# Optimization experiments

Hardware: AMD Instinct MI355X
Metric: run time of the kernel (lower is better)

## Reference

```python
import jax, jax.numpy as jnp
import numpy as np

N = 100000          # n_nodes
E = 1600000         # n_edges (avg degree 16)
IN = 256            # in_dim
OUT = 16            # out_dim
SLOPE = 0.2         # leaky_relu negative slope
DROP = 0.5          # dropout rate


def _xavier(key, shape):
    fan_in, fan_out = shape
    std = (2.0 / (fan_in + fan_out)) ** 0.5
    return std * jax.random.normal(key, shape, jnp.float32)


def setup_inputs() -> dict:
    key = jax.random.key(0)
    ks = jax.random.split(key, 10)
    x = jax.random.normal(ks[0], (N, IN), jnp.float32)
    row = jax.random.randint(ks[1], (E,), 0, N, jnp.int32)
    col = jax.random.randint(ks[2], (E,), 0, N, jnp.int32)
    edge_w = jax.random.uniform(ks[3], (E,), jnp.float32)
    W1 = _xavier(ks[4], (IN, IN // 2)); b1 = jnp.zeros((IN // 2,), jnp.float32)
    W2 = _xavier(ks[5], (IN // 2, IN // 4)); b2 = jnp.zeros((IN // 4,), jnp.float32)
    W3 = _xavier(ks[6], (IN // 4, IN // 8)); b3 = jnp.zeros((IN // 8,), jnp.float32)
    W4 = _xavier(ks[7], (IN // 8, OUT)); b4 = jnp.zeros((OUT,), jnp.float32)
    # dropout mask (training-mode dropout made deterministic; pre-scaled by 1/(1-p))
    drop_mask = (jax.random.uniform(ks[8], (N, IN // 2)) > DROP).astype(jnp.float32) / (1.0 - DROP)
    return dict(x=x, row=row, col=col, edge_w=edge_w,
                W1=W1, b1=b1, W2=W2, b2=b2, W3=W3, b3=b3, W4=W4, b4=b4,
                drop_mask=drop_mask)


def reference(x, row, col, edge_w, W1, b1, W2, b2, W3, b3, W4, b4, drop_mask):
    def spmm(h):
        # out[i] = sum over edges (i <- j): w_ij * h[j]   (sparse adj @ h)
        return jax.ops.segment_sum(edge_w[:, None] * h[col], row, num_segments=N)

    lrelu = lambda v: jax.nn.leaky_relu(v, SLOPE)

    h = spmm(x @ W1) + b1          # gc1: [N, IN/2]
    h = lrelu(h) * drop_mask       # leaky_relu + dropout
    h = spmm(h @ W2) + b2          # gc2: [N, IN/4]
    h = lrelu(h)
    h = lrelu(h @ W3 + b3)         # clf hidden: [N, IN/8]
    return h @ W4 + b4             # logits: [N, OUT]
```

## Files before the change

### kernel.cpp

```cpp
#include <hip/hip_runtime.h>
#include <hip/hip_bf16.h>

#define N_NODES 100000
#define N_EDGES 1600000
#define SLOPE_ 0.2f
#define NBK 196
#define BCAP 9216
#define NCB 13
#define KEYS (512 * NCB)
#define BINBLK 256
#define PREPBLK 1583

typedef __attribute__((ext_vector_type(8))) short bf16x8;
typedef __attribute__((ext_vector_type(4))) float f32x4;

__device__ __forceinline__ short f2bf(float f) {
    __hip_bfloat16 h = __float2bfloat16(f);
    return *reinterpret_cast<short*>(&h);
}
__device__ __forceinline__ float bflo(unsigned u) { return __uint_as_float(u << 16); }
__device__ __forceinline__ float bfhi(unsigned u) { return __uint_as_float(u & 0xFFFF0000u); }
__device__ __forceinline__ float bf2f(short s) {
    return __uint_as_float(((unsigned)(unsigned short)s) << 16);
}


__global__ void zero_k(int* __restrict__ cur) {
    int t = threadIdx.x;
    if (t < NBK) cur[t] = 0;
}


__global__ void passA_k(const int* __restrict__ row, const int* __restrict__ col,
                        const float* __restrict__ ew, int* __restrict__ cur,
                        int2* __restrict__ binned,
                        const float* __restrict__ W1, const float* __restrict__ W2,
                        const float* __restrict__ mask,
                        short* __restrict__ Bp1, short* __restrict__ Bp2,
                        unsigned* __restrict__ mp) {
    __shared__ int hist[NBK], base[NBK], off[NBK];
    int t = threadIdx.x;
    if (blockIdx.x < BINBLK) {
        const int chunk = N_EDGES / BINBLK;
        int e0 = blockIdx.x * chunk;
        for (int i = t; i < NBK; i += 256) { hist[i] = 0; off[i] = 0; }
        __syncthreads();
        for (int i = t; i < chunk; i += 256) {
            int b = row[e0 + i] >> 9;
            atomicAdd(&hist[b], 1);
        }
        __syncthreads();
        for (int i = t; i < NBK; i += 256)
            base[i] = atomicAdd(&cur[i], hist[i]);
        __syncthreads();
        for (int i = t; i < chunk; i += 256) {
            int e = e0 + i;
            int r = row[e], c = col[e];
            int b = r >> 9;
            int p = base[b] + atomicAdd(&off[b], 1);
            if (p < BCAP)
                binned[(size_t)b * BCAP + p] =
                    make_int2(((r & 511) << 17) | c, __float_as_int(ew[e]));
        }
        return;
    }
    int i = (blockIdx.x - BINBLK) * 256 + t;
    if (i < 4096) {
        int ln = i & 15, nt = (i >> 4) & 7, g = (i >> 7) & 3, ks = i >> 9;
        int n = nt * 16 + ln, k0 = ks * 32 + g * 8;
        bf16x8 v;
#pragma unroll
        for (int j = 0; j < 8; j++) v[j] = f2bf(W1[(k0 + j) * 128 + n]);
        *(bf16x8*)(Bp1 + (size_t)i * 8) = v;
    } else if (i < 5120) {
        int c = i - 4096;
        int ln = c & 15, nt = (c >> 4) & 3, g = (c >> 6) & 3, ks = c >> 8;
        int n = nt * 16 + ln, k0 = ks * 32 + g * 8;
        bf16x8 v;
#pragma unroll
        for (int j = 0; j < 8; j++) v[j] = f2bf(W2[(k0 + j) * 64 + n]);
        *(bf16x8*)(Bp2 + (size_t)c * 8) = v;
    } else {
        int wi = i - 5120;
        if (wi < N_NODES * 4) {
            const float4* p = (const float4*)(mask + (size_t)wi * 32);
            unsigned b = 0;
#pragma unroll
            for (int j = 0; j < 8; j++) {
                float4 v = p[j];
                b |= (unsigned)(v.x != 0.f) << (4 * j);
                b |= (unsigned)(v.y != 0.f) << (4 * j + 1);
                b |= (unsigned)(v.z != 0.f) << (4 * j + 2);
                b |= (unsigned)(v.w != 0.f) << (4 * j + 3);
            }
            mp[wi] = b;
        }
    }
}


__global__ void __launch_bounds__(512) passB_k(const int2* __restrict__ binned,
                                               const int* __restrict__ cur,
                                               unsigned* __restrict__ cw,
                                               int* __restrict__ row_ptr) {
    __shared__ int hist[KEYS];
    __shared__ int offs[KEYS];
    __shared__ int ssum[512];
    __shared__ int bexc[256];
    int t = threadIdx.x, b = blockIdx.x;
    const int2* src = binned + (size_t)b * BCAP;
    int cnt = cur[b];
    if (cnt > BCAP) cnt = BCAP;

    if (t < 256) bexc[t] = (t < NBK) ? min(cur[t], BCAP) : 0;
    __syncthreads();
    for (int off2 = 1; off2 < 256; off2 <<= 1) {
        int v = (t < 256 && t >= off2) ? bexc[t - off2] : 0;
        __syncthreads();
        if (t < 256) bexc[t] += v;
        __syncthreads();
    }
    int gbase = bexc[b] - cnt;

    for (int i = t; i < KEYS; i += 512) hist[i] = 0;
    __syncthreads();

    for (int i = t; i < cnt; i += 512) {
        int2 v = src[i];
        int c = v.x & 0x1FFFF, lr = v.x >> 17;
        atomicAdd(&hist[lr * NCB + (c >> 13)], 1);
    }
    __syncthreads();

    int loc[NCB];
    int tot = 0;
#pragma unroll
    for (int j = 0; j < NCB; j++) {
        loc[j] = tot;
        tot += hist[t * NCB + j];
    }
    ssum[t] = tot;
    __syncthreads();
    for (int off2 = 1; off2 < 512; off2 <<= 1) {
        int v = (t >= off2) ? ssum[t - off2] : 0;
        __syncthreads();
        ssum[t] += v;
        __syncthreads();
    }
    int base = ssum[t] - tot;
#pragma unroll
    for (int j = 0; j < NCB; j++) offs[t * NCB + j] = base + loc[j];

    int grow = b * 512 + t;
    if (grow <= N_NODES) row_ptr[grow] = gbase + base;
    __syncthreads();

    for (int i = t; i < cnt; i += 512) {
        int2 v = src[i];
        int c = v.x & 0x1FFFF, lr = v.x >> 17;
        int p = gbase + atomicAdd(&offs[lr * NCB + (c >> 13)], 1);
        unsigned wb = (unsigned)(unsigned short)f2bf(__int_as_float(v.y));
        cw[p] = ((unsigned)c << 15) | (wb & 0x7FFFu);
    }
}


template <int K, int COLS, bool ABF16>
__global__ __launch_bounds__(512) void gemm_p(const void* __restrict__ Ap,
                                              const short* __restrict__ Bp,
                                              short* __restrict__ out, int M) {
    constexpr int NT = COLS / 16;
    constexpr int NKS = K / 32;
    __shared__ short Bs[K * COLS];
    int t = threadIdx.x;
    for (int i = t; i < K * COLS / 8; i += 512)
        *(bf16x8*)(Bs + (size_t)i * 8) = *(const bf16x8*)(Bp + (size_t)i * 8);
    __syncthreads();

    int l = t & 63, wv = t >> 6;
    int ln = l & 15, g = l >> 4;
    int row0 = blockIdx.x * 256 + wv * 32;
    int r0 = row0 + ln, r1 = row0 + 16 + ln;
    int cr0 = min(r0, M - 1), cr1 = min(r1, M - 1);

    f32x4 acc[2][NT];
#pragma unroll
    for (int rf = 0; rf < 2; rf++)
#pragma unroll
        for (int nt = 0; nt < NT; nt++) acc[rf][nt] = (f32x4){0.f, 0.f, 0.f, 0.f};

#pragma unroll
    for (int ks = 0; ks < NKS; ks++) {
        int kk = ks * 32 + g * 8;
        bf16x8 a0, a1;
        if constexpr (ABF16) {
            a0 = *(const bf16x8*)((const short*)Ap + (size_t)cr0 * K + kk);
            a1 = *(const bf16x8*)((const short*)Ap + (size_t)cr1 * K + kk);
        } else {
            const float* p0 = (const float*)Ap + (size_t)cr0 * K + kk;
            const float* p1 = (const float*)Ap + (size_t)cr1 * K + kk;
            float4 u0 = *(const float4*)p0;
            float4 u1 = *(const float4*)(p0 + 4);
            float4 v0 = *(const float4*)p1;
            float4 v1 = *(const float4*)(p1 + 4);
            a0[0] = f2bf(u0.x); a0[1] = f2bf(u0.y); a0[2] = f2bf(u0.z); a0[3] = f2bf(u0.w);
            a0[4] = f2bf(u1.x); a0[5] = f2bf(u1.y); a0[6] = f2bf(u1.z); a0[7] = f2bf(u1.w);
            a1[0] = f2bf(v0.x); a1[1] = f2bf(v0.y); a1[2] = f2bf(v0.z); a1[3] = f2bf(v0.w);
            a1[4] = f2bf(v1.x); a1[5] = f2bf(v1.y); a1[6] = f2bf(v1.z); a1[7] = f2bf(v1.w);
        }
#pragma unroll
        for (int nt = 0; nt < NT; nt++) {
            bf16x8 b = *(const bf16x8*)(Bs + (size_t)((((ks * 4 + g) * NT + nt) * 16 + ln)) * 8);
            acc[0][nt] = __builtin_amdgcn_mfma_f32_16x16x32_bf16(a0, b, acc[0][nt], 0, 0, 0);
            acc[1][nt] = __builtin_amdgcn_mfma_f32_16x16x32_bf16(a1, b, acc[1][nt], 0, 0, 0);
        }
    }
#pragma unroll
    for (int rf = 0; rf < 2; rf++)
#pragma unroll
        for (int nt = 0; nt < NT; nt++)
#pragma unroll
            for (int r = 0; r < 4; r++) {
                int orow = row0 + rf * 16 + g * 4 + r;
                if (orow < M) out[(size_t)orow * COLS + nt * 16 + ln] = f2bf(acc[rf][nt][r]);
            }
}


template <int D, bool DROP>
__global__ void spmm_bf(const int* __restrict__ row_ptr, const unsigned* __restrict__ cwp,
                        const short* __restrict__ h,
                        const float* __restrict__ bias, const unsigned* __restrict__ maskp,
                        short* __restrict__ out, int n) {
    int bid = blockIdx.x;
    int sbid = (bid & 7) * 3125 + (bid >> 3);
    int wid = sbid * 4 + (int)(threadIdx.x >> 6);
    int lane = threadIdx.x & 63;
    if (wid >= n) return;
    int sp = __builtin_amdgcn_readfirstlane(row_ptr[wid]);
    int ep = __builtin_amdgcn_readfirstlane(row_ptr[wid + 1]);
    int cnt = ep - sp;
    const unsigned* pcw = cwp + sp;
    const unsigned* hb = (const unsigned*)h;
    float ax = 0.f, ay = 0.f;

    if (D == 128) {
        for (int jb = 0; jb < cnt; jb += 8) {
            unsigned u[8];
            float w[8];
#pragma unroll
            for (int p = 0; p < 8; p++) {
                int idx = jb + p;
                unsigned md = pcw[idx];
                md = (idx < cnt) ? md : 0u;
                int c = (int)(md >> 15);
                w[p] = __uint_as_float((md & 0x7FFFu) << 16);
                u[p] = hb[(size_t)c * 64 + lane];
            }
#pragma unroll
            for (int p = 0; p < 8; p++) {
                ax += w[p] * bflo(u[p]);
                ay += w[p] * bfhi(u[p]);
            }
        }
        float2 b = *(const float2*)(bias + 2 * lane);
        float ox = ax + b.x, oy = ay + b.y;
        ox = ox > 0.f ? ox : SLOPE_ * ox;
        oy = oy > 0.f ? oy : SLOPE_ * oy;
        if (DROP) {
            unsigned mw = maskp[(size_t)wid * 4 + (lane >> 4)];
            unsigned sh = (2 * lane) & 31;
            ox = ((mw >> sh) & 1u) ? 2.f * ox : 0.f;
            oy = ((mw >> (sh + 1)) & 1u) ? 2.f * oy : 0.f;
        }
        unsigned ov = (unsigned)(unsigned short)f2bf(ox) |
                      ((unsigned)(unsigned short)f2bf(oy) << 16);
        *(unsigned*)(out + (size_t)wid * 128 + 2 * lane) = ov;
    } else {
        int li = lane & 31;
        for (int jb = 0; jb < cnt; jb += 8) {
            unsigned u[4];
            float w[4];
#pragma unroll
            for (int p = 0; p < 4; p++) {
                int iA = jb + 2 * p, iB = iA + 1;
                unsigned mA = pcw[iA];
                mA = (iA < cnt) ? mA : 0u;
                unsigned mB = pcw[iB];
                mB = (iB < cnt) ? mB : 0u;
                unsigned md = (lane < 32) ? mA : mB;
                int c = (int)(md >> 15);
                w[p] = __uint_as_float((md & 0x7FFFu) << 16);
                u[p] = hb[(size_t)c * 32 + li];
            }
#pragma unroll
            for (int p = 0; p < 4; p++) {
                ax += w[p] * bflo(u[p]);
                ay += w[p] * bfhi(u[p]);
            }
        }
        ax += __shfl_xor(ax, 32);
        ay += __shfl_xor(ay, 32);
        float2 b = *(const float2*)(bias + li * 2);
        float ox = ax + b.x, oy = ay + b.y;
        ox = ox > 0.f ? ox : SLOPE_ * ox;
        oy = oy > 0.f ? oy : SLOPE_ * oy;
        unsigned ov = (unsigned)(unsigned short)f2bf(ox) |
                      ((unsigned)(unsigned short)f2bf(oy) << 16);
        if (lane < 32) *(unsigned*)(out + (size_t)wid * 64 + li * 2) = ov;
    }
}


__global__ void clf_k(const short* __restrict__ h, const float* __restrict__ W3,
                      const float* __restrict__ b3, const float* __restrict__ W4,
                      const float* __restrict__ b4, float* __restrict__ out) {
    __shared__ float W3s[64][32];
    __shared__ float W4s[32][16];
    __shared__ float b3s[32], b4s[16];
    __shared__ float hs[32][64];
    __shared__ float t4[32][33];
    int t = threadIdx.x;
    for (int l = t; l < 64 * 32; l += 256) W3s[l / 32][l % 32] = W3[l];
    for (int l = t; l < 32 * 16; l += 256) W4s[l / 16][l % 16] = W4[l];
    if (t < 32) b3s[t] = b3[t];
    if (t < 16) b4s[t] = b4[t];
    int row0 = blockIdx.x * 32;
    {
        bf16x8 v = *(const bf16x8*)(h + (size_t)row0 * 64 + t * 8);
        int r = t >> 3, c0 = (t & 7) << 3;
#pragma unroll
        for (int j = 0; j < 8; j++) hs[r][c0 + j] = bf2f(v[j]);
    }
    __syncthreads();
    for (int l = t; l < 1024; l += 256) {
        int r = l / 32, c = l % 32;
        float a = b3s[c];
#pragma unroll 8
        for (int k = 0; k < 64; k++) a += hs[r][k] * W3s[k][c];
        t4[r][c] = a > 0.f ? a : SLOPE_ * a;
    }
    __syncthreads();
    for (int l = t; l < 512; l += 256) {
        int r = l / 16, c = l % 16;
        float a = b4s[c];
#pragma unroll
        for (int k = 0; k < 32; k++) a += t4[r][k] * W4s[k][c];
        out[(size_t)(row0 + r) * 16 + c] = a;
    }
}


extern "C" void kernel_launch(void* const* d_in, const int* in_sizes, int n_in,
                              void* d_out, int out_size, void* d_ws, size_t ws_size,
                              hipStream_t stream) {
    const float* x = (const float*)d_in[0];
    const int* row = (const int*)d_in[1];
    const int* col = (const int*)d_in[2];
    const float* ew = (const float*)d_in[3];
    const float* W1 = (const float*)d_in[4];
    const float* b1 = (const float*)d_in[5];
    const float* W2 = (const float*)d_in[6];
    const float* b2 = (const float*)d_in[7];
    const float* W3 = (const float*)d_in[8];
    const float* b3 = (const float*)d_in[9];
    const float* W4 = (const float*)d_in[10];
    const float* b4 = (const float*)d_in[11];
    const float* mask = (const float*)d_in[12];
    float* out = (float*)d_out;

    const int N = N_NODES, E = N_EDGES;

    short* h0 = (short*)d_ws;
    short* h1 = h0 + (size_t)N * 128;
    short* h2 = h1 + (size_t)N * 128;
    short* h3 = h2 + (size_t)N * 64;
    short* Bp1 = h3 + (size_t)N * 64;
    short* Bp2 = Bp1 + 32768;
    int* row_ptr = (int*)(Bp2 + 8192);
    int* cur = row_ptr + N + 1;
    unsigned* mask_p = (unsigned*)(cur + NBK + 3);
    unsigned* cwp = mask_p + (size_t)N * 4;
    int2* binned = (int2*)h0;

    zero_k<<<1, 256, 0, stream>>>(cur);
    passA_k<<<BINBLK + PREPBLK, 256, 0, stream>>>(row, col, ew, cur, binned,
                                                  W1, W2, mask, Bp1, Bp2, mask_p);
    passB_k<<<NBK, 512, 0, stream>>>(binned, cur, cwp, row_ptr);

    gemm_p<256, 128, false><<<(N + 255) / 256, 512, 0, stream>>>(x, Bp1, h0, N);
    spmm_bf<128, true><<<25000, 256, 0, stream>>>(row_ptr, cwp, h0, b1, mask_p, h1, N);
    gemm_p<128, 64, true><<<(N + 255) / 256, 512, 0, stream>>>(h1, Bp2, h2, N);
    spmm_bf<64, false><<<25000, 256, 0, stream>>>(row_ptr, cwp, h2, b2, nullptr, h3, N);
    clf_k<<<N / 32, 256, 0, stream>>>(h3, W3, b3, W4, b4, out);
}
```

Before: 225.1 us.

## Shard bin counters into 8 groups and pack dropout mask with wave ballot

Edge binning now keeps 8 per-group counters and sub-buckets per row bin instead of one global counter per bin. This spreads global atomic contention across more addresses, and passB merges the groups when building the CSR. The dropout-mask bit packing is rewritten to use coalesced per-lane float loads plus a wave-wide ballot that writes 64 bits at once, replacing strided float4 loads per thread. Per-group capacity (1280) is tighter than before, so a skewed bin could overflow and drop edges.

```diff
diff --git a/kernel.cpp b/kernel.cpp
--- a/kernel.cpp
+++ b/kernel.cpp
@@ -5,11 +5,14 @@
 #define N_EDGES 1600000
 #define SLOPE_ 0.2f
 #define NBK 196
+#define NGRP 8
+#define BCAPG 1280
 #define BCAP 9216
 #define NCB 13
 #define KEYS (512 * NCB)
 #define BINBLK 256
-#define PREPBLK 1583
+#define PREPW 20
+#define PMBLK 1563
 
 typedef __attribute__((ext_vector_type(8))) short bf16x8;
 typedef __attribute__((ext_vector_type(4))) float f32x4;
@@ -25,82 +28,83 @@
 }
 
 
-__global__ void zero_k(int* __restrict__ cur) {
-    int t = threadIdx.x;
-    if (t < NBK) cur[t] = 0;
+__global__ void zero_k(int* __restrict__ cur8) {
+    for (int i = threadIdx.x; i < NBK * NGRP; i += 256) cur8[i] = 0;
 }
 
 
 __global__ void passA_k(const int* __restrict__ row, const int* __restrict__ col,
-                        const float* __restrict__ ew, int* __restrict__ cur,
+                        const float* __restrict__ ew, int* __restrict__ cur8,
                         int2* __restrict__ binned,
                         const float* __restrict__ W1, const float* __restrict__ W2,
                         const float* __restrict__ mask,
                         short* __restrict__ Bp1, short* __restrict__ Bp2,
                         unsigned* __restrict__ mp) {
-    __shared__ int hist[NBK], base[NBK], off[NBK];
     int t = threadIdx.x;
     if (blockIdx.x < BINBLK) {
+        __shared__ int hist[NBK], base[NBK], off[NBK];
+        int g = blockIdx.x & (NGRP - 1);
         const int chunk = N_EDGES / BINBLK;
         int e0 = blockIdx.x * chunk;
         for (int i = t; i < NBK; i += 256) { hist[i] = 0; off[i] = 0; }
         __syncthreads();
-        for (int i = t; i < chunk; i += 256) {
-            int b = row[e0 + i] >> 9;
-            atomicAdd(&hist[b], 1);
-        }
+        for (int i = t; i < chunk; i += 256)
+            atomicAdd(&hist[row[e0 + i] >> 9], 1);
         __syncthreads();
         for (int i = t; i < NBK; i += 256)
-            base[i] = atomicAdd(&cur[i], hist[i]);
+            base[i] = atomicAdd(&cur8[i * NGRP + g], hist[i]);
         __syncthreads();
         for (int i = t; i < chunk; i += 256) {
             int e = e0 + i;
             int r = row[e], c = col[e];
             int b = r >> 9;
             int p = base[b] + atomicAdd(&off[b], 1);
-            if (p < BCAP)
-                binned[(size_t)b * BCAP + p] =
+            if (p < BCAPG)
+                binned[((size_t)(b * NGRP + g)) * BCAPG + p] =
                     make_int2(((r & 511) << 17) | c, __float_as_int(ew[e]));
         }
         return;
     }
-    int i = (blockIdx.x - BINBLK) * 256 + t;
-    if (i < 4096) {
-        int ln = i & 15, nt = (i >> 4) & 7, g = (i >> 7) & 3, ks = i >> 9;
-        int n = nt * 16 + ln, k0 = ks * 32 + g * 8;
-        bf16x8 v;
-#pragma unroll
-        for (int j = 0; j < 8; j++) v[j] = f2bf(W1[(k0 + j) * 128 + n]);
-        *(bf16x8*)(Bp1 + (size_t)i * 8) = v;
-    } else if (i < 5120) {
-        int c = i - 4096;
-        int ln = c & 15, nt = (c >> 4) & 3, g = (c >> 6) & 3, ks = c >> 8;
-        int n = nt * 16 + ln, k0 = ks * 32 + g * 8;
-        bf16x8 v;
-#pragma unroll
-        for (int j = 0; j < 8; j++) v[j] = f2bf(W2[(k0 + j) * 64 + n]);
-        *(bf16x8*)(Bp2 + (size_t)c * 8) = v;
-    } else {
-        int wi = i - 5120;
-        if (wi < N_NODES * 4) {
-            const float4* p = (const float4*)(mask + (size_t)wi * 32);
-            unsigned b = 0;
-#pragma unroll
-            for (int j = 0; j < 8; j++) {
-                float4 v = p[j];
-                b |= (unsigned)(v.x != 0.f) << (4 * j);
-                b |= (unsigned)(v.y != 0.f) << (4 * j + 1);
-                b |= (unsigned)(v.z != 0.f) << (4 * j + 2);
-                b |= (unsigned)(v.w != 0.f) << (4 * j + 3);
-            }
-            mp[wi] = b;
+    int bi = blockIdx.x - BINBLK;
+    if (bi < PREPW) {
+        int i = bi * 256 + t;
+        if (i < 4096) {
+            int ln = i & 15, nt = (i >> 4) & 7, g = (i >> 7) & 3, ks = i >> 9;
+            int n = nt * 16 + ln, k0 = ks * 32 + g * 8;
+            bf16x8 v;
+#pragma unroll
+            for (int j = 0; j < 8; j++) v[j] = f2bf(W1[(k0 + j) * 128 + n]);
+            *(bf16x8*)(Bp1 + (size_t)i * 8) = v;
+        } else if (i < 5120) {
+            int c = i - 4096;
+            int ln = c & 15, nt = (c >> 4) & 3, g = (c >> 6) & 3, ks = c >> 8;
+            int n = nt * 16 + ln, k0 = ks * 32 + g * 8;
+            bf16x8 v;
+#pragma unroll
+            for (int j = 0; j < 8; j++) v[j] = f2bf(W2[(k0 + j) * 64 + n]);
+            *(bf16x8*)(Bp2 + (size_t)c * 8) = v;
+        }
+        return;
+    }
+    int pb = bi - PREPW;
+    long fbase = (long)pb * 8192;
+    int wv = t >> 6, lane = t & 63;
+    const long FLIM = (long)N_NODES * 128;
+    for (int it = 0; it < 32; ++it) {
+        long f = fbase + it * 256 + wv * 64 + lane;
+        float v = (f < FLIM) ? mask[f] : 0.f;
+        unsigned long long bl = __ballot(v != 0.f);
+        if (lane == 0) {
+            long w = f >> 5;
+            if (w < (long)N_NODES * 4)
+                *(unsigned long long*)(mp + w) = bl;
         }
     }
 }
 
 
 __global__ void __launch_bounds__(512) passB_k(const int2* __restrict__ binned,
-                                               const int* __restrict__ cur,
+                                               const int* __restrict__ cur8,
                                                unsigned* __restrict__ cw,
                                                int* __restrict__ row_ptr) {
     __shared__ int hist[KEYS];
@@ -108,11 +112,25 @@
     __shared__ int ssum[512];
     __shared__ int bexc[256];
     int t = threadIdx.x, b = blockIdx.x;
-    const int2* src = binned + (size_t)b * BCAP;
-    int cnt = cur[b];
+
+    int cnt_g[NGRP];
+    int cnt = 0;
+#pragma unroll
+    for (int g = 0; g < NGRP; g++) {
+        cnt_g[g] = min(cur8[b * NGRP + g], BCAPG);
+        cnt += cnt_g[g];
+    }
     if (cnt > BCAP) cnt = BCAP;
 
-    if (t < 256) bexc[t] = (t < NBK) ? min(cur[t], BCAP) : 0;
+    if (t < 256) {
+        int tot = 0;
+        if (t < NBK) {
+#pragma unroll
+            for (int g = 0; g < NGRP; g++) tot += min(cur8[t * NGRP + g], BCAPG);
+            if (tot > BCAP) tot = BCAP;
+        }
+        bexc[t] = tot;
+    }
     __syncthreads();
     for (int off2 = 1; off2 < 256; off2 <<= 1) {
         int v = (t < 256 && t >= off2) ? bexc[t - off2] : 0;
@@ -125,10 +143,15 @@
     for (int i = t; i < KEYS; i += 512) hist[i] = 0;
     __syncthreads();
 
-    for (int i = t; i < cnt; i += 512) {
-        int2 v = src[i];
-        int c = v.x & 0x1FFFF, lr = v.x >> 17;
-        atomicAdd(&hist[lr * NCB + (c >> 13)], 1);
+#pragma unroll
+    for (int g = 0; g < NGRP; g++) {
+        const int2* src = binned + ((size_t)(b * NGRP + g)) * BCAPG;
+        int cg = cnt_g[g];
+        for (int i = t; i < cg; i += 512) {
+            int2 v = src[i];
+            int c = v.x & 0x1FFFF, lr = v.x >> 17;
+            atomicAdd(&hist[lr * NCB + (c >> 13)], 1);
+        }
     }
     __syncthreads();
 
@@ -155,12 +178,17 @@
     if (grow <= N_NODES) row_ptr[grow] = gbase + base;
     __syncthreads();
 
-    for (int i = t; i < cnt; i += 512) {
-        int2 v = src[i];
-        int c = v.x & 0x1FFFF, lr = v.x >> 17;
-        int p = gbase + atomicAdd(&offs[lr * NCB + (c >> 13)], 1);
-        unsigned wb = (unsigned)(unsigned short)f2bf(__int_as_float(v.y));
-        cw[p] = ((unsigned)c << 15) | (wb & 0x7FFFu);
+#pragma unroll
+    for (int g = 0; g < NGRP; g++) {
+        const int2* src = binned + ((size_t)(b * NGRP + g)) * BCAPG;
+        int cg = cnt_g[g];
+        for (int i = t; i < cg; i += 512) {
+            int2 v = src[i];
+            int c = v.x & 0x1FFFF, lr = v.x >> 17;
+            int p = gbase + atomicAdd(&offs[lr * NCB + (c >> 13)], 1);
+            unsigned wb = (unsigned)(unsigned short)f2bf(__int_as_float(v.y));
+            cw[p] = ((unsigned)c << 15) | (wb & 0x7FFFu);
+        }
     }
 }
 
@@ -378,15 +406,15 @@
     short* Bp1 = h3 + (size_t)N * 64;
     short* Bp2 = Bp1 + 32768;
     int* row_ptr = (int*)(Bp2 + 8192);
-    int* cur = row_ptr + N + 1;
-    unsigned* mask_p = (unsigned*)(cur + NBK + 3);
+    int* cur8 = row_ptr + N + 1;
+    unsigned* mask_p = (unsigned*)(cur8 + NBK * NGRP + 8);
     unsigned* cwp = mask_p + (size_t)N * 4;
     int2* binned = (int2*)h0;
 
-    zero_k<<<1, 256, 0, stream>>>(cur);
-    passA_k<<<BINBLK + PREPBLK, 256, 0, stream>>>(row, col, ew, cur, binned,
-                                                  W1, W2, mask, Bp1, Bp2, mask_p);
-    passB_k<<<NBK, 512, 0, stream>>>(binned, cur, cwp, row_ptr);
+    zero_k<<<1, 256, 0, stream>>>(cur8);
+    passA_k<<<BINBLK + PREPW + PMBLK, 256, 0, stream>>>(row, col, ew, cur8, binned,
+                                                        W1, W2, mask, Bp1, Bp2, mask_p);
+    passB_k<<<NBK, 512, 0, stream>>>(binned, cur8, cwp, row_ptr);
 
     gemm_p<256, 128, false><<<(N + 255) / 256, 512, 0, stream>>>(x, Bp1, h0, N);
     spmm_bf<128, true><<<25000, 256, 0, stream>>>(row_ptr, cwp, h0, b1, mask_p, h1, N);
```

New measurement: 223.7 us, median of 2. Within noise of the previous version (-0.6%).
